# Optimization experiments

Measured on AMD Instinct MI355X. Metric: run time of the kernel, lower is better.

The kernel has to match this reference:

```python
import jax, jax.numpy as jnp
import numpy as np

B, T, C, H = 4, 2048, 1024, 16
D = C // H  # head_size = 64


def setup_inputs() -> dict:
    key = jax.random.key(0)
    k1, k2, k3 = jax.random.split(key, 3)
    x = jax.random.normal(k1, (B, T, C), dtype=jnp.float32)
    w_qkv = jax.random.normal(k2, (C, 3 * C), dtype=jnp.float32) * (C ** -0.5)
    b_qkv = jnp.zeros((3 * C,), dtype=jnp.float32)
    w_proj = jax.random.normal(k3, (C, C), dtype=jnp.float32) * (C ** -0.5)
    b_proj = jnp.zeros((C,), dtype=jnp.float32)
    return {"x": x, "w_qkv": w_qkv, "b_qkv": b_qkv, "w_proj": w_proj, "b_proj": b_proj}


def reference(x, w_qkv, b_qkv, w_proj, b_proj):
    b, t, c = x.shape
    qkv = x @ w_qkv + b_qkv                      # [B,T,3C]
    q, k, v = jnp.split(qkv, 3, axis=-1)
    # [B,T,C] -> [B,H,T,D]
    q = q.reshape(b, t, H, D).transpose(0, 2, 1, 3)
    k = k.reshape(b, t, H, D).transpose(0, 2, 1, 3)
    v = v.reshape(b, t, H, D).transpose(0, 2, 1, 3)
    attn = jnp.einsum('bhqd,bhkd->bhqk', q, k) * (D ** -0.5)
    causal = jnp.tril(jnp.ones((t, t), dtype=bool))
    attn = jnp.where(causal[None, None], attn, -jnp.inf)
    attn = jax.nn.softmax(attn, axis=-1)
    # dropout: eval mode (identity)
    out = jnp.einsum('bhqk,bhkd->bhqd', attn, v)
    out = out.transpose(0, 2, 1, 3).reshape(b, t, c)
    return out @ w_proj + b_proj
```

## Files before the change

### kernel.cpp

```cpp
#include <hip/hip_runtime.h>

#define B_ 4
#define T_ 2048
#define C_ 1024
#define H_ 16
#define D_ 64

typedef __attribute__((ext_vector_type(8))) short short8;
typedef __attribute__((ext_vector_type(4))) float f32x4;

__device__ inline unsigned short f2bf(float f) {
    union { float f; unsigned u; } v; v.f = f;
    unsigned r = v.u + 0x7fffu + ((v.u >> 16) & 1u);
    return (unsigned short)(r >> 16);
}

__device__ inline unsigned int pk_bf16(float a, float b) {
#if __has_builtin(__builtin_amdgcn_cvt_pk_bf16_f32)
    typedef __attribute__((ext_vector_type(2))) __bf16 bf16x2;
    bf16x2 v = __builtin_amdgcn_cvt_pk_bf16_f32(a, b);
    return __builtin_bit_cast(unsigned int, v);
#else
    return (unsigned)f2bf(a) | ((unsigned)f2bf(b) << 16);
#endif
}

__device__ inline float dpp_max16(float x) {
    int t;
    t = __builtin_amdgcn_update_dpp(0, __builtin_bit_cast(int, x), 0xB1, 0xF, 0xF, true);
    x = fmaxf(x, __builtin_bit_cast(float, t));
    t = __builtin_amdgcn_update_dpp(0, __builtin_bit_cast(int, x), 0x4E, 0xF, 0xF, true);
    x = fmaxf(x, __builtin_bit_cast(float, t));
    t = __builtin_amdgcn_update_dpp(0, __builtin_bit_cast(int, x), 0x141, 0xF, 0xF, true);
    x = fmaxf(x, __builtin_bit_cast(float, t));
    t = __builtin_amdgcn_update_dpp(0, __builtin_bit_cast(int, x), 0x140, 0xF, 0xF, true);
    x = fmaxf(x, __builtin_bit_cast(float, t));
    return x;
}

__device__ inline void async_ld16(const void* g, void* lds) {
    __builtin_amdgcn_global_load_lds(
        (const __attribute__((address_space(1))) unsigned int*)g,
        (__attribute__((address_space(3))) unsigned int*)lds, 16, 0, 0);
}

__global__ __launch_bounds__(256) void prep_all(
    const float* __restrict__ x, const float* __restrict__ w_qkv,
    const float* __restrict__ w_proj,
    unsigned short* __restrict__ xb, unsigned short* __restrict__ wqkvT,
    unsigned short* __restrict__ wprojT)
{
    const int bid = blockIdx.x;
    if (bid < 8192) {
        int i = (bid * 256 + threadIdx.x) * 4;
        float4 v = *(const float4*)(x + i);
        uint2 o;
        o.x = pk_bf16(v.x, v.y);
        o.y = pk_bf16(v.z, v.w);
        *(uint2*)(xb + i) = o;
        return;
    }
    __shared__ float tile[32][33];
    const int tt = bid - 8192;
    int bx = tt & 127;
    const int by = tt >> 7;
    const float* src; unsigned short* dst; int Cc;
    if (bx < 96) { src = w_qkv;  dst = wqkvT;  Cc = 3072; }
    else         { src = w_proj; dst = wprojT; Cc = 1024; bx -= 96; }
    const int tx = threadIdx.x & 31, ty = threadIdx.x >> 5;
    #pragma unroll
    for (int r = 0; r < 32; r += 8)
        tile[ty + r][tx] = src[(size_t)(by*32 + ty + r) * Cc + bx*32 + tx];
    __syncthreads();
    #pragma unroll
    for (int r = 0; r < 32; r += 8)
        dst[(size_t)(bx*32 + ty + r) * 1024 + by*32 + tx] = f2bf(tile[tx][ty + r]);
}

__global__ __launch_bounds__(256) void gemm_qkv(
    const unsigned short* __restrict__ A,
    const unsigned short* __restrict__ BT,
    const float* __restrict__ bias,
    unsigned short* __restrict__ qb, unsigned short* __restrict__ kb,
    unsigned short* __restrict__ vtb)
{
    __shared__ unsigned short As0[128 * 32], As1[128 * 32];
    __shared__ unsigned short Bs0[128 * 32], Bs1[128 * 32];
    const int tid = threadIdx.x;
    const int wave = tid >> 6, lane = tid & 63;
    const int wm = wave >> 1, wn = wave & 1;
    const int l15 = lane & 15, lq = lane >> 4;
    const int m0 = blockIdx.y * 128, n0 = blockIdx.x * 128;
    const int srow = tid >> 2, sg = tid & 3;
    const int sel = n0 >> 10;

    f32x4 acc[4][4] = {};

    for (int k0 = 0; k0 < 1024; k0 += 64) {
        #pragma unroll
        for (int r = 0; r < 2; ++r) {
            const size_t ra = (size_t)(m0 + r*64 + srow) * 1024 + k0 + sg*8;
            const size_t rb = (size_t)(n0 + r*64 + srow) * 1024 + k0 + sg*8;
            async_ld16(A  + ra,      (char*)As0 + r*4096 + wave*1024);
            async_ld16(A  + ra + 32, (char*)As1 + r*4096 + wave*1024);
            async_ld16(BT + rb,      (char*)Bs0 + r*4096 + wave*1024);
            async_ld16(BT + rb + 32, (char*)Bs1 + r*4096 + wave*1024);
        }
        __syncthreads();
        #pragma unroll
        for (int ks = 0; ks < 2; ++ks) {
            const unsigned short* Asx = ks ? As1 : As0;
            const unsigned short* Bsx = ks ? Bs1 : Bs0;
            short8 af[4], bf[4];
            #pragma unroll
            for (int i = 0; i < 4; ++i) {
                af[i] = *(const short8*)&Asx[(wm*64 + i*16 + l15) * 32 + lq*8];
                bf[i] = *(const short8*)&Bsx[(wn*64 + i*16 + l15) * 32 + lq*8];
            }
            if (sel < 2) {
                #pragma unroll
                for (int mi = 0; mi < 4; ++mi)
                    #pragma unroll
                    for (int ni = 0; ni < 4; ++ni)
                        acc[mi][ni] = __builtin_amdgcn_mfma_f32_16x16x32_bf16(
                            bf[ni], af[mi], acc[mi][ni], 0, 0, 0);
            } else {
                #pragma unroll
                for (int mi = 0; mi < 4; ++mi)
                    #pragma unroll
                    for (int ni = 0; ni < 4; ++ni)
                        acc[mi][ni] = __builtin_amdgcn_mfma_f32_16x16x32_bf16(
                            af[mi], bf[ni], acc[mi][ni], 0, 0, 0);
            }
        }
        __syncthreads();
    }

    if (sel < 2) {
        const float qs = (sel == 0) ? 0.180336880f : 1.0f;
        unsigned short* dst = (sel == 0) ? qb : kb;
        #pragma unroll
        for (int mi = 0; mi < 4; ++mi) {
            const int t = m0 + wm*64 + mi*16 + l15;
            const int bb = t >> 11, tt = t & 2047;
            #pragma unroll
            for (int ni = 0; ni < 4; ++ni) {
                const int nb = n0 + wn*64 + ni*16 + lq*4;
                const int hh = (nb >> 6) & 15, d0 = nb & 63;
                float4 bv = *(const float4*)(bias + nb);
                float v0 = (acc[mi][ni][0] + bv.x) * qs;
                float v1 = (acc[mi][ni][1] + bv.y) * qs;
                float v2 = (acc[mi][ni][2] + bv.z) * qs;
                float v3 = (acc[mi][ni][3] + bv.w) * qs;
                uint2 pk; pk.x = pk_bf16(v0, v1); pk.y = pk_bf16(v2, v3);
                *(uint2*)(dst + ((size_t)(bb*16 + hh)*2048 + tt)*64 + d0) = pk;
            }
        }
    } else {
        #pragma unroll
        for (int mi = 0; mi < 4; ++mi) {
            const int t0 = m0 + wm*64 + mi*16 + lq*4;
            const int bb = t0 >> 11, tt = t0 & 2047;
            #pragma unroll
            for (int ni = 0; ni < 4; ++ni) {
                const int n = n0 + wn*64 + ni*16 + l15;
                const int hh = (n >> 6) & 15, d = n & 63;
                const float bs = bias[n];
                uint2 pk;
                pk.x = pk_bf16(acc[mi][ni][0] + bs, acc[mi][ni][1] + bs);
                pk.y = pk_bf16(acc[mi][ni][2] + bs, acc[mi][ni][3] + bs);
                *(uint2*)(vtb + ((size_t)(bb*16 + hh)*64 + d)*2048 + tt) = pk;
            }
        }
    }
}

__global__ __launch_bounds__(256) void gemm_proj(
    const unsigned short* __restrict__ A,
    const unsigned short* __restrict__ BT,
    const float* __restrict__ bias,
    float* __restrict__ out)
{
    __shared__ unsigned short As0[128 * 32], As1[128 * 32];
    __shared__ unsigned short Bs0[128 * 32], Bs1[128 * 32];
    const int tid = threadIdx.x;
    const int wave = tid >> 6, lane = tid & 63;
    const int wm = wave >> 1, wn = wave & 1;
    const int l15 = lane & 15, lq = lane >> 4;
    const int m0 = blockIdx.y * 128, n0 = blockIdx.x * 128;
    const int srow = tid >> 2, sg = tid & 3;

    f32x4 acc[4][4] = {};

    for (int k0 = 0; k0 < 1024; k0 += 64) {
        #pragma unroll
        for (int r = 0; r < 2; ++r) {
            const size_t ra = (size_t)(m0 + r*64 + srow) * 1024 + k0 + sg*8;
            const size_t rb = (size_t)(n0 + r*64 + srow) * 1024 + k0 + sg*8;
            async_ld16(A  + ra,      (char*)As0 + r*4096 + wave*1024);
            async_ld16(A  + ra + 32, (char*)As1 + r*4096 + wave*1024);
            async_ld16(BT + rb,      (char*)Bs0 + r*4096 + wave*1024);
            async_ld16(BT + rb + 32, (char*)Bs1 + r*4096 + wave*1024);
        }
        __syncthreads();
        #pragma unroll
        for (int ks = 0; ks < 2; ++ks) {
            const unsigned short* Asx = ks ? As1 : As0;
            const unsigned short* Bsx = ks ? Bs1 : Bs0;
            short8 af[4], bf[4];
            #pragma unroll
            for (int i = 0; i < 4; ++i) {
                af[i] = *(const short8*)&Asx[(wm*64 + i*16 + l15) * 32 + lq*8];
                bf[i] = *(const short8*)&Bsx[(wn*64 + i*16 + l15) * 32 + lq*8];
            }
            #pragma unroll
            for (int mi = 0; mi < 4; ++mi)
                #pragma unroll
                for (int ni = 0; ni < 4; ++ni)
                    acc[mi][ni] = __builtin_amdgcn_mfma_f32_16x16x32_bf16(
                        bf[ni], af[mi], acc[mi][ni], 0, 0, 0);
        }
        __syncthreads();
    }

    #pragma unroll
    for (int mi = 0; mi < 4; ++mi) {
        const int m = m0 + wm*64 + mi*16 + l15;
        #pragma unroll
        for (int ni = 0; ni < 4; ++ni) {
            const int nb = n0 + wn*64 + ni*16 + lq*4;
            float4 bv = *(const float4*)(bias + nb);
            float4 o;
            o.x = acc[mi][ni][0] + bv.x;
            o.y = acc[mi][ni][1] + bv.y;
            o.z = acc[mi][ni][2] + bv.z;
            o.w = acc[mi][ni][3] + bv.w;
            *(float4*)(out + (size_t)m * 1024 + nb) = o;
        }
    }
}

__global__ __launch_bounds__(256, 5) void attn_mfma(
    const unsigned short* __restrict__ qb,
    const unsigned short* __restrict__ kb,
    const unsigned short* __restrict__ vtb,
    unsigned short* __restrict__ ab)
{
    __shared__ unsigned short Ks[64][72];
    __shared__ unsigned short Vt[80][72];
    __shared__ unsigned short Ps[64][72];

    const int tid  = threadIdx.x;
    const int wave = tid >> 6, lane = tid & 63;
    const int l15  = lane & 15, lq = lane >> 4;
    const int linear = blockIdx.x;
    const int xc  = linear & 7;
    const int idx = linear >> 3;
    const int bh  = xc * 8 + (idx & 7);
    const int qblk = 31 - (idx >> 3);
    const int q0 = qblk * 64;
    const int b = bh >> 4, h = bh & 15;
    const size_t base = (size_t)bh * 2048 * 64;

    for (int i = tid; i < 16 * 72; i += 256) {
        int r = i / 72, cc = i - r * 72;
        Vt[64 + r][cc] = (r == 0) ? (unsigned short)0x3F80 : (unsigned short)0;
    }
    #pragma unroll
    for (int i = 0; i < 2; ++i) {
        int slot = tid + 256 * i;
        int row = slot >> 3, g = slot & 7;
        *(uint4*)&Ps[row][g*8] = *(const uint4*)(qb + base + (size_t)(q0 + row)*64 + g*8);
    }
    __syncthreads();
    short8 qf[2];
    qf[0] = *(const short8*)&Ps[wave*16 + l15][lq*8];
    qf[1] = *(const short8*)&Ps[wave*16 + l15][32 + lq*8];

    f32x4 o[4] = {}, lac = {};
    float mrow[4] = {-1e30f, -1e30f, -1e30f, -1e30f};

    for (int j0 = 0; j0 <= q0; j0 += 64) {
        __syncthreads();
        #pragma unroll
        for (int i = 0; i < 2; ++i) {
            int slot = tid + 256 * i;
            int row = slot >> 3, g = slot & 7;
            *(uint4*)&Ks[row][g*8] = *(const uint4*)(kb  + base + (size_t)(j0 + row)*64 + g*8);
            *(uint4*)&Vt[row][g*8] = *(const uint4*)(vtb + base + (size_t)row*2048 + j0 + g*8);
        }
        __syncthreads();

        f32x4 s[4] = {};
        #pragma unroll
        for (int ks = 0; ks < 2; ++ks)
            #pragma unroll
            for (int ni = 0; ni < 4; ++ni) {
                short8 kf = *(const short8*)&Ks[ni*16 + l15][ks*32 + lq*8];
                s[ni] = __builtin_amdgcn_mfma_f32_16x16x32_bf16(qf[ks], kf, s[ni], 0, 0, 0);
            }

        if (j0 == q0) {
            #pragma unroll
            for (int ni = 0; ni < 4; ++ni) {
                int kc = ni*16 + l15;
                #pragma unroll
                for (int r = 0; r < 4; ++r) {
                    int qr = wave*16 + lq*4 + r;
                    if (kc > qr) s[ni][r] = -1e30f;
                }
            }
        }

        float al[4];
        #pragma unroll
        for (int r = 0; r < 4; ++r) {
            float mx = fmaxf(fmaxf(s[0][r], s[1][r]), fmaxf(s[2][r], s[3][r]));
            mx = dpp_max16(mx);
            float mnew = fmaxf(mrow[r], mx);
            al[r] = __builtin_amdgcn_exp2f(mrow[r] - mnew);
            mrow[r] = mnew;
        }
        #pragma unroll
        for (int r = 0; r < 4; ++r) {
            float p0 = __builtin_amdgcn_exp2f(s[0][r] - mrow[r]);
            float p1 = __builtin_amdgcn_exp2f(s[1][r] - mrow[r]);
            float p2 = __builtin_amdgcn_exp2f(s[2][r] - mrow[r]);
            float p3 = __builtin_amdgcn_exp2f(s[3][r] - mrow[r]);
            unsigned pa = pk_bf16(p0, p1), pb = pk_bf16(p2, p3);
            const int row = wave*16 + lq*4 + r;
            Ps[row][l15]      = (unsigned short)pa;
            Ps[row][16 + l15] = (unsigned short)(pa >> 16);
            Ps[row][32 + l15] = (unsigned short)pb;
            Ps[row][48 + l15] = (unsigned short)(pb >> 16);
            o[0][r] *= al[r]; o[1][r] *= al[r];
            o[2][r] *= al[r]; o[3][r] *= al[r];
            lac[r] *= al[r];
        }

        #pragma unroll
        for (int ks = 0; ks < 2; ++ks) {
            short8 pf = *(const short8*)&Ps[wave*16 + l15][ks*32 + lq*8];
            #pragma unroll
            for (int ni = 0; ni < 4; ++ni) {
                short8 vf = *(const short8*)&Vt[ni*16 + l15][ks*32 + lq*8];
                o[ni] = __builtin_amdgcn_mfma_f32_16x16x32_bf16(pf, vf, o[ni], 0, 0, 0);
            }
            short8 vl = *(const short8*)&Vt[64 + l15][ks*32 + lq*8];
            lac = __builtin_amdgcn_mfma_f32_16x16x32_bf16(pf, vl, lac, 0, 0, 0);
        }
    }

    #pragma unroll
    for (int r = 0; r < 4; ++r) {
        float l = __shfl(lac[r], (lane & 48));
        float linv = __builtin_amdgcn_rcpf(l);
        int m = b*2048 + q0 + wave*16 + lq*4 + r;
        unsigned pa = pk_bf16(o[0][r]*linv, o[1][r]*linv);
        unsigned pb = pk_bf16(o[2][r]*linv, o[3][r]*linv);
        unsigned short* p = ab + (size_t)m*1024 + h*64;
        p[l15]      = (unsigned short)pa;
        p[16 + l15] = (unsigned short)(pa >> 16);
        p[32 + l15] = (unsigned short)pb;
        p[48 + l15] = (unsigned short)(pb >> 16);
    }
}

extern "C" void kernel_launch(void* const* d_in, const int* in_sizes, int n_in,
                              void* d_out, int out_size, void* d_ws, size_t ws_size,
                              hipStream_t stream) {
    const float* x      = (const float*)d_in[0];
    const float* w_qkv  = (const float*)d_in[1];
    const float* b_qkv  = (const float*)d_in[2];
    const float* w_proj = (const float*)d_in[3];
    const float* b_proj = (const float*)d_in[4];
    float* out = (float*)d_out;

    unsigned short* xb     = (unsigned short*)d_ws;
    unsigned short* wqkvT  = xb + 8388608;
    unsigned short* wprojT = wqkvT + 3145728;
    unsigned short* qbuf   = wprojT + 1048576;
    unsigned short* kbuf   = qbuf + 8388608;
    unsigned short* vtbuf  = kbuf + 8388608;
    unsigned short* abuf   = vtbuf + 8388608;

    prep_all<<<12288, 256, 0, stream>>>(x, w_qkv, w_proj, xb, wqkvT, wprojT);
    gemm_qkv<<<dim3(24, 64), 256, 0, stream>>>(xb, wqkvT, b_qkv, qbuf, kbuf, vtbuf);
    attn_mfma<<<2048, 256, 0, stream>>>(qbuf, kbuf, vtbuf, abuf);
    gemm_proj<<<dim3(8, 64), 256, 0, stream>>>(abuf, wprojT, b_proj, out);
}
```

Before: 266.1 us.

## Double attention query tile per block and register-prefetch next K/V tile

Each attention block now handles 128 query rows (32 per wave, two 16-row MFMA tiles), so every K/V tile loaded into shared memory feeds twice the work and the grid halves to 1024 blocks. Q fragments are read straight from global memory into registers instead of staging through LDS. The next K/V tile is loaded into registers while the current one is computed, and waves whose rows are fully masked skip the compute. In exchange it uses more registers (occupancy hint lowered from 5 to 4) and causal imbalance inside a block grows, since some waves sit idle on the last tile.

```diff
diff --git a/kernel.cpp b/kernel.cpp
--- a/kernel.cpp
+++ b/kernel.cpp
@@ -240,7 +240,7 @@
     }
 }
 
-__global__ __launch_bounds__(256, 5) void attn_mfma(
+__global__ __launch_bounds__(256, 4) void attn_mfma(
     const unsigned short* __restrict__ qb,
     const unsigned short* __restrict__ kb,
     const unsigned short* __restrict__ vtb,
@@ -248,7 +248,7 @@
 {
     __shared__ unsigned short Ks[64][72];
     __shared__ unsigned short Vt[80][72];
-    __shared__ unsigned short Ps[64][72];
+    __shared__ unsigned short Ps[128][72];
 
     const int tid  = threadIdx.x;
     const int wave = tid >> 6, lane = tid & 63;
@@ -257,8 +257,8 @@
     const int xc  = linear & 7;
     const int idx = linear >> 3;
     const int bh  = xc * 8 + (idx & 7);
-    const int qblk = 31 - (idx >> 3);
-    const int q0 = qblk * 64;
+    const int qblk = 15 - (idx >> 3);
+    const int q0 = qblk * 128;
     const int b = bh >> 4, h = bh & 15;
     const size_t base = (size_t)bh * 2048 * 64;
 
@@ -266,104 +266,144 @@
         int r = i / 72, cc = i - r * 72;
         Vt[64 + r][cc] = (r == 0) ? (unsigned short)0x3F80 : (unsigned short)0;
     }
-    #pragma unroll
-    for (int i = 0; i < 2; ++i) {
-        int slot = tid + 256 * i;
-        int row = slot >> 3, g = slot & 7;
-        *(uint4*)&Ps[row][g*8] = *(const uint4*)(qb + base + (size_t)(q0 + row)*64 + g*8);
-    }
-    __syncthreads();
-    short8 qf[2];
-    qf[0] = *(const short8*)&Ps[wave*16 + l15][lq*8];
-    qf[1] = *(const short8*)&Ps[wave*16 + l15][32 + lq*8];
-
-    f32x4 o[4] = {}, lac = {};
-    float mrow[4] = {-1e30f, -1e30f, -1e30f, -1e30f};
-
-    for (int j0 = 0; j0 <= q0; j0 += 64) {
-        __syncthreads();
+
+    short8 qf[2][2];
+    #pragma unroll
+    for (int mi = 0; mi < 2; ++mi)
+        #pragma unroll
+        for (int ks = 0; ks < 2; ++ks)
+            qf[mi][ks] = *(const short8*)(qb + base +
+                (size_t)(q0 + wave*32 + mi*16 + l15)*64 + ks*32 + lq*8);
+
+    uint4 kr[2], vr[2];
+    {
         #pragma unroll
         for (int i = 0; i < 2; ++i) {
             int slot = tid + 256 * i;
             int row = slot >> 3, g = slot & 7;
-            *(uint4*)&Ks[row][g*8] = *(const uint4*)(kb  + base + (size_t)(j0 + row)*64 + g*8);
-            *(uint4*)&Vt[row][g*8] = *(const uint4*)(vtb + base + (size_t)row*2048 + j0 + g*8);
-        }
-        __syncthreads();
-
-        f32x4 s[4] = {};
+            kr[i] = *(const uint4*)(kb  + base + (size_t)row*64 + g*8);
+            vr[i] = *(const uint4*)(vtb + base + (size_t)row*2048 + g*8);
+        }
+    }
+
+    f32x4 o[2][4] = {};
+    f32x4 lac[2] = {};
+    float mrow[2][4];
+    #pragma unroll
+    for (int mi = 0; mi < 2; ++mi)
+        #pragma unroll
+        for (int r = 0; r < 4; ++r) mrow[mi][r] = -1e30f;
+
+    const int wq_lo = q0 + wave * 32;
+    const int wq_hi = wq_lo + 31;
+    const int jmax  = q0 + 64;
+
+    for (int j0 = 0; j0 <= jmax; j0 += 64) {
+        __syncthreads();
+        #pragma unroll
+        for (int i = 0; i < 2; ++i) {
+            int slot = tid + 256 * i;
+            int row = slot >> 3, g = slot & 7;
+            *(uint4*)&Ks[row][g*8] = kr[i];
+            *(uint4*)&Vt[row][g*8] = vr[i];
+        }
+        __syncthreads();
+
+        if (j0 + 64 <= jmax) {
+            #pragma unroll
+            for (int i = 0; i < 2; ++i) {
+                int slot = tid + 256 * i;
+                int row = slot >> 3, g = slot & 7;
+                kr[i] = *(const uint4*)(kb  + base + (size_t)(j0 + 64 + row)*64 + g*8);
+                vr[i] = *(const uint4*)(vtb + base + (size_t)row*2048 + j0 + 64 + g*8);
+            }
+        }
+        if (j0 > wq_hi) continue;
+
+        f32x4 s[2][4] = {};
         #pragma unroll
         for (int ks = 0; ks < 2; ++ks)
             #pragma unroll
             for (int ni = 0; ni < 4; ++ni) {
                 short8 kf = *(const short8*)&Ks[ni*16 + l15][ks*32 + lq*8];
-                s[ni] = __builtin_amdgcn_mfma_f32_16x16x32_bf16(qf[ks], kf, s[ni], 0, 0, 0);
-            }
-
-        if (j0 == q0) {
-            #pragma unroll
-            for (int ni = 0; ni < 4; ++ni) {
-                int kc = ni*16 + l15;
+                s[0][ni] = __builtin_amdgcn_mfma_f32_16x16x32_bf16(qf[0][ks], kf, s[0][ni], 0, 0, 0);
+                s[1][ni] = __builtin_amdgcn_mfma_f32_16x16x32_bf16(qf[1][ks], kf, s[1][ni], 0, 0, 0);
+            }
+
+        if (j0 + 63 > wq_lo) {
+            #pragma unroll
+            for (int mi = 0; mi < 2; ++mi)
                 #pragma unroll
-                for (int r = 0; r < 4; ++r) {
-                    int qr = wave*16 + lq*4 + r;
-                    if (kc > qr) s[ni][r] = -1e30f;
-                }
-            }
-        }
-
-        float al[4];
-        #pragma unroll
-        for (int r = 0; r < 4; ++r) {
-            float mx = fmaxf(fmaxf(s[0][r], s[1][r]), fmaxf(s[2][r], s[3][r]));
-            mx = dpp_max16(mx);
-            float mnew = fmaxf(mrow[r], mx);
-            al[r] = __builtin_amdgcn_exp2f(mrow[r] - mnew);
-            mrow[r] = mnew;
-        }
-        #pragma unroll
-        for (int r = 0; r < 4; ++r) {
-            float p0 = __builtin_amdgcn_exp2f(s[0][r] - mrow[r]);
-            float p1 = __builtin_amdgcn_exp2f(s[1][r] - mrow[r]);
-            float p2 = __builtin_amdgcn_exp2f(s[2][r] - mrow[r]);
-            float p3 = __builtin_amdgcn_exp2f(s[3][r] - mrow[r]);
-            unsigned pa = pk_bf16(p0, p1), pb = pk_bf16(p2, p3);
-            const int row = wave*16 + lq*4 + r;
-            Ps[row][l15]      = (unsigned short)pa;
-            Ps[row][16 + l15] = (unsigned short)(pa >> 16);
-            Ps[row][32 + l15] = (unsigned short)pb;
-            Ps[row][48 + l15] = (unsigned short)(pb >> 16);
-            o[0][r] *= al[r]; o[1][r] *= al[r];
-            o[2][r] *= al[r]; o[3][r] *= al[r];
-            lac[r] *= al[r];
+                for (int ni = 0; ni < 4; ++ni)
+                    #pragma unroll
+                    for (int r = 0; r < 4; ++r) {
+                        int qr = wq_lo + mi*16 + lq*4 + r;
+                        int kc = j0 + ni*16 + l15;
+                        if (kc > qr) s[mi][ni][r] = -1e30f;
+                    }
+        }
+
+        #pragma unroll
+        for (int mi = 0; mi < 2; ++mi) {
+            float al[4];
+            #pragma unroll
+            for (int r = 0; r < 4; ++r) {
+                float mx = fmaxf(fmaxf(s[mi][0][r], s[mi][1][r]),
+                                 fmaxf(s[mi][2][r], s[mi][3][r]));
+                mx = dpp_max16(mx);
+                float mnew = fmaxf(mrow[mi][r], mx);
+                al[r] = __builtin_amdgcn_exp2f(mrow[mi][r] - mnew);
+                mrow[mi][r] = mnew;
+            }
+            #pragma unroll
+            for (int r = 0; r < 4; ++r) {
+                float p0 = __builtin_amdgcn_exp2f(s[mi][0][r] - mrow[mi][r]);
+                float p1 = __builtin_amdgcn_exp2f(s[mi][1][r] - mrow[mi][r]);
+                float p2 = __builtin_amdgcn_exp2f(s[mi][2][r] - mrow[mi][r]);
+                float p3 = __builtin_amdgcn_exp2f(s[mi][3][r] - mrow[mi][r]);
+                unsigned pa = pk_bf16(p0, p1), pb = pk_bf16(p2, p3);
+                const int row = wave*32 + mi*16 + lq*4 + r;
+                Ps[row][l15]      = (unsigned short)pa;
+                Ps[row][16 + l15] = (unsigned short)(pa >> 16);
+                Ps[row][32 + l15] = (unsigned short)pb;
+                Ps[row][48 + l15] = (unsigned short)(pb >> 16);
+                o[mi][0][r] *= al[r]; o[mi][1][r] *= al[r];
+                o[mi][2][r] *= al[r]; o[mi][3][r] *= al[r];
+                lac[mi][r] *= al[r];
+            }
         }
 
         #pragma unroll
         for (int ks = 0; ks < 2; ++ks) {
-            short8 pf = *(const short8*)&Ps[wave*16 + l15][ks*32 + lq*8];
+            short8 pf0 = *(const short8*)&Ps[wave*32 +      l15][ks*32 + lq*8];
+            short8 pf1 = *(const short8*)&Ps[wave*32 + 16 + l15][ks*32 + lq*8];
             #pragma unroll
             for (int ni = 0; ni < 4; ++ni) {
                 short8 vf = *(const short8*)&Vt[ni*16 + l15][ks*32 + lq*8];
-                o[ni] = __builtin_amdgcn_mfma_f32_16x16x32_bf16(pf, vf, o[ni], 0, 0, 0);
+                o[0][ni] = __builtin_amdgcn_mfma_f32_16x16x32_bf16(pf0, vf, o[0][ni], 0, 0, 0);
+                o[1][ni] = __builtin_amdgcn_mfma_f32_16x16x32_bf16(pf1, vf, o[1][ni], 0, 0, 0);
             }
             short8 vl = *(const short8*)&Vt[64 + l15][ks*32 + lq*8];
-            lac = __builtin_amdgcn_mfma_f32_16x16x32_bf16(pf, vl, lac, 0, 0, 0);
-        }
-    }
-
-    #pragma unroll
-    for (int r = 0; r < 4; ++r) {
-        float l = __shfl(lac[r], (lane & 48));
-        float linv = __builtin_amdgcn_rcpf(l);
-        int m = b*2048 + q0 + wave*16 + lq*4 + r;
-        unsigned pa = pk_bf16(o[0][r]*linv, o[1][r]*linv);
-        unsigned pb = pk_bf16(o[2][r]*linv, o[3][r]*linv);
-        unsigned short* p = ab + (size_t)m*1024 + h*64;
-        p[l15]      = (unsigned short)pa;
-        p[16 + l15] = (unsigned short)(pa >> 16);
-        p[32 + l15] = (unsigned short)pb;
-        p[48 + l15] = (unsigned short)(pb >> 16);
-    }
+            lac[0] = __builtin_amdgcn_mfma_f32_16x16x32_bf16(pf0, vl, lac[0], 0, 0, 0);
+            lac[1] = __builtin_amdgcn_mfma_f32_16x16x32_bf16(pf1, vl, lac[1], 0, 0, 0);
+        }
+    }
+
+    #pragma unroll
+    for (int mi = 0; mi < 2; ++mi)
+        #pragma unroll
+        for (int r = 0; r < 4; ++r) {
+            float l = __shfl(lac[mi][r], (lane & 48));
+            float linv = __builtin_amdgcn_rcpf(l);
+            int m = b*2048 + q0 + wave*32 + mi*16 + lq*4 + r;
+            unsigned pa = pk_bf16(o[mi][0][r]*linv, o[mi][1][r]*linv);
+            unsigned pb = pk_bf16(o[mi][2][r]*linv, o[mi][3][r]*linv);
+            unsigned short* p = ab + (size_t)m*1024 + h*64;
+            p[l15]      = (unsigned short)pa;
+            p[16 + l15] = (unsigned short)(pa >> 16);
+            p[32 + l15] = (unsigned short)pb;
+            p[48 + l15] = (unsigned short)(pb >> 16);
+        }
 }
 
 extern "C" void kernel_launch(void* const* d_in, const int* in_sizes, int n_in,
@@ -386,6 +426,6 @@
 
     prep_all<<<12288, 256, 0, stream>>>(x, w_qkv, w_proj, xb, wqkvT, wprojT);
     gemm_qkv<<<dim3(24, 64), 256, 0, stream>>>(xb, wqkvT, b_qkv, qbuf, kbuf, vtbuf);
-    attn_mfma<<<2048, 256, 0, stream>>>(qbuf, kbuf, vtbuf, abuf);
+    attn_mfma<<<1024, 256, 0, stream>>>(qbuf, kbuf, vtbuf, abuf);
     gemm_proj<<<dim3(8, 64), 256, 0, stream>>>(abuf, wprojT, b_proj, out);
 }
```

New measurement: 303.7 us. 14.1% more time.
